# Optimization experiments

Measured on AMD Instinct MI355X. Metric: run time of the kernel, lower is better.

Reference implementation:

```python
import jax, jax.numpy as jnp
import numpy as np

NUM_EDGES = 500_000
FEAT_DIM = 128
TIME_DIM = 100
OUT_DIM = 128
NUM_TYPES = 4


def setup_inputs() -> dict:
    key = jax.random.key(0)
    k1, k2, k3, k4, k5, k6 = jax.random.split(key, 6)
    edge_feats = jax.random.normal(k1, (NUM_EDGES, FEAT_DIM), dtype=jnp.float32)
    edge_ts = jax.random.uniform(k2, (NUM_EDGES,), dtype=jnp.float32) * 100.0
    edge_types = jax.random.randint(k3, (NUM_EDGES,), 0, NUM_TYPES, dtype=jnp.int32)
    # per-type linear encoders: Linear(time_dim + feat_dim, out_dim)
    in_dim = TIME_DIM + FEAT_DIM
    W = jax.random.normal(k4, (NUM_TYPES, in_dim, OUT_DIM), dtype=jnp.float32) * (1.0 / np.sqrt(in_dim))
    b = jax.random.normal(k5, (NUM_TYPES, OUT_DIM), dtype=jnp.float32) * 0.02
    type_emb = jax.random.normal(k6, (NUM_TYPES, OUT_DIM), dtype=jnp.float32)
    # frozen per-type time frequencies: base 1/10**linspace(0,9,T) scaled by (1 + 0.1*i)
    base = (1.0 / 10 ** np.linspace(0, 9, TIME_DIM, dtype=np.float32))
    mult = (1.0 + 0.1 * np.arange(NUM_TYPES, dtype=np.float32))[:, None]
    freqs = jnp.asarray(base[None, :] * mult)  # [T, time_dim]
    return {"edge_feats": edge_feats, "edge_ts": edge_ts, "edge_types": edge_types,
            "W": W, "b": b, "type_emb": type_emb, "freqs": freqs}


def reference(edge_feats, edge_ts, edge_types, W, b, type_emb, freqs):
    # Hetero time encode: cos(t * freq_per_type), bias is zero (frozen)
    time_emb = jnp.cos(edge_ts[:, None] * freqs[edge_types])  # [E, time_dim]
    combined = jnp.concatenate([edge_feats, time_emb], axis=1)  # [E, time+feat]
    num_types = W.shape[0]
    out = jnp.zeros((combined.shape[0], W.shape[2]), dtype=edge_feats.dtype)
    # per-edge-type masked dispatch to separate linear encoders, scatter combine
    for i in range(num_types):
        yi = combined @ W[i] + b[i] + type_emb[i]  # [E, out_dim]
        out = jnp.where((edge_types == i)[:, None], yi, out)
    return out
```

## Files before the change

### kernel.cpp

```cpp
#include <hip/hip_runtime.h>
#include <hip/hip_bf16.h>
#include <cstdint>
#include <cstddef>

#define E_N 500000
#define FD 128
#define TD 100
#define OD 128
#define NT 4
#define IND 228
#define KP 256
#define GX 256
#define NB 1954

static constexpr size_t BUCKET_OFF = 0;
static constexpr size_t WBF_OFF    = 2000000;
static constexpr size_t BIASC_OFF  = WBF_OFF + (size_t)NT * OD * KP * 2;
static constexpr size_t CTR_OFF    = BIASC_OFF + (size_t)NT * OD * 4;
static constexpr size_t PART_OFF   = CTR_OFF + 64;
static constexpr size_t BBASE_OFF  = PART_OFF + (size_t)NB * 4 * 4;
static constexpr size_t WS_NEED    = BBASE_OFF + (size_t)NB * 4 * 4;

typedef __attribute__((ext_vector_type(8))) short short8;
typedef __attribute__((ext_vector_type(4))) float f32x4;

__device__ __forceinline__ unsigned short f2bf(float x) {
  union { float f; unsigned u; } v; v.f = x;
  unsigned r = v.u + 0x7fff + ((v.u >> 16) & 1);
  return (unsigned short)(r >> 16);
}

__device__ __forceinline__ unsigned pack2bf(float a, float b) {
  union { __hip_bfloat162 h; unsigned u; } c;
  c.h = __float22bfloat162_rn(make_float2(a, b));
  return c.u;
}

__device__ __forceinline__ int a_off(int r, int k) {
  return ((r << 9) + (k << 1)) ^ ((r & 7) << 4);
}

__global__ void hist_kernel(const int* __restrict__ types, int* __restrict__ partial, int n) {
  __shared__ int wcnt[4][NT];
  const int tid = threadIdx.x, w = tid >> 6, l = tid & 63;
  const int i = blockIdx.x * 256 + tid;
  const int t = (i < n) ? types[i] : -1;
  #pragma unroll
  for (int q = 0; q < NT; ++q) {
    unsigned long long m = __ballot(t == q);
    if (l == 0) wcnt[w][q] = (int)__popcll(m);
  }
  __syncthreads();
  if (tid < NT) {
    int s = 0;
    #pragma unroll
    for (int w2 = 0; w2 < 4; ++w2) s += wcnt[w2][tid];
    partial[blockIdx.x * NT + tid] = s;
  }
}

__global__ void scan_kernel(const int* __restrict__ partial, int* __restrict__ blockbase,
                            int* __restrict__ ctr, const float* __restrict__ b,
                            const float* __restrict__ temb, float* __restrict__ biasc) {
  __shared__ int4 tsum[256];
  const int tid = threadIdx.x;
  int4 s = make_int4(0, 0, 0, 0);
  #pragma unroll
  for (int j = 0; j < 8; ++j) {
    int blk = tid * 8 + j;
    if (blk < NB) {
      const int* p = partial + blk * 4;
      s.x += p[0]; s.y += p[1]; s.z += p[2]; s.w += p[3];
    }
  }
  tsum[tid] = s;
  __syncthreads();
  if (tid == 0) {
    int4 run = make_int4(0, 0, 0, 0);
    for (int i = 0; i < 256; ++i) {
      int4 v = tsum[i]; tsum[i] = run;
      run.x += v.x; run.y += v.y; run.z += v.z; run.w += v.w;
    }
    ctr[0] = run.x; ctr[1] = run.y; ctr[2] = run.z; ctr[3] = run.w;
    int off = 0;
    ctr[4] = 0;            off += run.x;
    ctr[5] = off;          off += run.y;
    ctr[6] = off;          off += run.z;
    ctr[7] = off;
  }
  __syncthreads();
  int4 run = tsum[tid];
  #pragma unroll
  for (int j = 0; j < 8; ++j) {
    int blk = tid * 8 + j;
    if (blk < NB) {
      const int* p = partial + blk * 4;
      int* bb = blockbase + blk * 4;
      bb[0] = run.x; bb[1] = run.y; bb[2] = run.z; bb[3] = run.w;
      run.x += p[0]; run.y += p[1]; run.z += p[2]; run.w += p[3];
    }
  }
  for (int i = tid; i < NT * OD; i += 256) biasc[i] = b[i] + temb[i];
}

__global__ void wconv_kernel(const float* __restrict__ W, unsigned short* __restrict__ Wbf) {
  int row = blockIdx.x * 4 + (threadIdx.x >> 6);
  int t = row >> 7, n = row & 127;
  int k0 = (threadIdx.x & 63) << 2;
  ushort4 o;
  float v0 = (k0 + 0 < IND) ? W[((size_t)t * IND + k0 + 0) * OD + n] : 0.f;
  float v1 = (k0 + 1 < IND) ? W[((size_t)t * IND + k0 + 1) * OD + n] : 0.f;
  float v2 = (k0 + 2 < IND) ? W[((size_t)t * IND + k0 + 2) * OD + n] : 0.f;
  float v3 = (k0 + 3 < IND) ? W[((size_t)t * IND + k0 + 3) * OD + n] : 0.f;
  o.x = f2bf(v0); o.y = f2bf(v1); o.z = f2bf(v2); o.w = f2bf(v3);
  *(ushort4*)(Wbf + ((size_t)row << 8) + k0) = o;
}

__global__ void fill_kernel(const int* __restrict__ types, const int* __restrict__ blockbase,
                            const int* __restrict__ ctr, int* __restrict__ bucket, int n) {
  __shared__ int wcnt[4][NT];
  __shared__ int wbase[4][NT];
  const int tid = threadIdx.x, w = tid >> 6, l = tid & 63;
  const int i = blockIdx.x * 256 + tid;
  const int t = (i < n) ? types[i] : -1;
  unsigned long long m[NT];
  #pragma unroll
  for (int q = 0; q < NT; ++q) {
    m[q] = __ballot(t == q);
    if (l == 0) wcnt[w][q] = (int)__popcll(m[q]);
  }
  __syncthreads();
  if (tid < NT) {
    int q = tid, s = 0;
    #pragma unroll
    for (int w2 = 0; w2 < 4; ++w2) { wbase[w2][q] = s; s += wcnt[w2][q]; }
  }
  __syncthreads();
  if (t >= 0) {
    int rank = wbase[w][t] + (int)__popcll(m[t] & ((1ull << l) - 1ull));
    bucket[ctr[4 + t] + blockbase[blockIdx.x * 4 + t] + rank] = i;
  }
}

__global__ __launch_bounds__(256) void gemm_kernel(
    const float* __restrict__ feats, const float* __restrict__ ts,
    const float* __restrict__ freqs, const unsigned short* __restrict__ Wbf,
    const float* __restrict__ biasc, const int* __restrict__ bucket,
    const int* __restrict__ ctr, float* __restrict__ out) {
  __shared__ __align__(16) char smA[64 * 512];
  __shared__ __align__(16) float sfreq[128];

  const int t = blockIdx.x;
  const int cnt = ctr[t];
  const int off = ctr[4 + t];
  const int ntiles = (cnt + 63) >> 6;
  const int chunk = (ntiles + GX - 1) / GX;
  const int t0 = blockIdx.y * chunk;
  const int t1 = min(t0 + chunk, ntiles);
  if (t0 >= t1) return;

  const int tid = threadIdx.x;
  const int wid = tid >> 6, lane = tid & 63;
  const int bl = lane & 15, bh = lane >> 4;
  const int r = tid >> 2, part = tid & 3;

  short8 bfrag[8][2];
  #pragma unroll
  for (int n = 0; n < 2; ++n) {
    const unsigned short* bp =
        Wbf + (((size_t)t * OD + wid * 32 + n * 16 + bl) << 8) + (bh << 3);
    #pragma unroll
    for (int k = 0; k < 8; ++k) bfrag[k][n] = *(const short8*)(bp + k * 32);
  }
  const float4 bv0 = *(const float4*)(biasc + t * OD + wid * 32 + bh * 4);
  const float4 bv1 = *(const float4*)(biasc + t * OD + wid * 32 + 16 + bh * 4);

  if (tid < 128) sfreq[tid] = (tid < TD) ? freqs[t * TD + tid] : 0.f;

  auto stage = [&](const float4* p, float tvv) {
    #pragma unroll
    for (int j = 0; j < 4; ++j) {
      uint4 q;
      q.x = pack2bf(p[2 * j].x, p[2 * j].y);
      q.y = pack2bf(p[2 * j].z, p[2 * j].w);
      q.z = pack2bf(p[2 * j + 1].x, p[2 * j + 1].y);
      q.w = pack2bf(p[2 * j + 1].z, p[2 * j + 1].w);
      *(uint4*)(smA + a_off(r, part * 32 + 8 * j)) = q;
    }
    #pragma unroll
    for (int j = 0; j < 4; ++j) {
      float4 f0 = *(const float4*)&sfreq[part * 32 + 8 * j];
      float4 f1 = *(const float4*)&sfreq[part * 32 + 8 * j + 4];
      uint4 q;
      q.x = pack2bf(__cosf(tvv * f0.x), __cosf(tvv * f0.y));
      q.y = pack2bf(__cosf(tvv * f0.z), __cosf(tvv * f0.w));
      q.z = pack2bf(__cosf(tvv * f1.x), __cosf(tvv * f1.y));
      q.w = pack2bf(__cosf(tvv * f1.z), __cosf(tvv * f1.w));
      *(uint4*)(smA + a_off(r, FD + part * 32 + 8 * j)) = q;
    }
  };

  int e_cur = -1; float tv_cur = 0.f;
  {
    const int va = min(64, cnt - t0 * 64);
    if (r < va) { e_cur = bucket[off + t0 * 64 + r]; tv_cur = ts[e_cur]; }
  }
  float4 pf[8];
  if (e_cur >= 0) {
    const float4* src = (const float4*)(feats + (size_t)e_cur * FD + part * 32);
    #pragma unroll
    for (int c = 0; c < 8; ++c) pf[c] = src[c];
  }
  int e_b = -1; float tv_b = 0.f;
  if (t0 + 1 < t1) {
    const int vb = min(64, cnt - (t0 + 1) * 64);
    if (r < vb) { e_b = bucket[off + (t0 + 1) * 64 + r]; tv_b = ts[e_b]; }
  }
  __syncthreads();
  if (e_cur >= 0) stage(pf, tv_cur);

  for (int tt = t0; tt < t1; ++tt) {
    const bool last = (tt == t1 - 1);
    __syncthreads();

    if (!last && e_b >= 0) {
      const float4* src = (const float4*)(feats + (size_t)e_b * FD + part * 32);
      #pragma unroll
      for (int c = 0; c < 8; ++c) pf[c] = src[c];
    }
    int e_c = -1; float tv_c = 0.f;
    if (tt + 2 < t1) {
      const int vc = min(64, cnt - (tt + 2) * 64);
      if (r < vc) { e_c = bucket[off + (tt + 2) * 64 + r]; tv_c = ts[e_c]; }
    }
    const int base = tt * 64;
    const int vcnt = cnt - base;
    int se[4];
    #pragma unroll
    for (int rt = 0; rt < 4; ++rt) {
      int rr = rt * 16 + bl;
      se[rt] = (rr < vcnt) ? bucket[off + base + rr] : -1;
    }

    __builtin_amdgcn_s_setprio(1);
    #pragma unroll
    for (int rt = 0; rt < 4; ++rt) {
      f32x4 a0, a1;
      a0[0] = bv0.x; a0[1] = bv0.y; a0[2] = bv0.z; a0[3] = bv0.w;
      a1[0] = bv1.x; a1[1] = bv1.y; a1[2] = bv1.z; a1[3] = bv1.w;
      #pragma unroll
      for (int k = 0; k < 8; ++k) {
        short8 av = *(const short8*)(smA + a_off(rt * 16 + bl, k * 32 + bh * 8));
        a0 = __builtin_amdgcn_mfma_f32_16x16x32_bf16(bfrag[k][0], av, a0, 0, 0, 0);
        a1 = __builtin_amdgcn_mfma_f32_16x16x32_bf16(bfrag[k][1], av, a1, 0, 0, 0);
      }
      if (se[rt] >= 0) {
        float* dst = out + (size_t)se[rt] * OD + wid * 32 + bh * 4;
        *(f32x4*)(dst)      = a0;
        *(f32x4*)(dst + 16) = a1;
      }
    }
    __builtin_amdgcn_s_setprio(0);
    __syncthreads();

    if (!last) {
      if (e_b >= 0) stage(pf, tv_b);
      e_cur = e_b; tv_cur = tv_b;
      e_b = e_c; tv_b = tv_c;
    }
  }
}

__global__ void naive_kernel(const float* __restrict__ feats, const float* __restrict__ ts,
                             const int* __restrict__ types, const float* __restrict__ W,
                             const float* __restrict__ b, const float* __restrict__ temb,
                             const float* __restrict__ freqs, float* __restrict__ out) {
  __shared__ float comb[IND];
  int e = blockIdx.x;
  int t = types[e];
  int tid = threadIdx.x;
  comb[tid] = feats[(size_t)e * FD + tid];
  if (tid < TD) comb[FD + tid] = __cosf(ts[e] * freqs[t * TD + tid]);
  __syncthreads();
  float acc = b[t * OD + tid] + temb[t * OD + tid];
  for (int k = 0; k < IND; ++k) acc += comb[k] * W[((size_t)t * IND + k) * OD + tid];
  out[(size_t)e * OD + tid] = acc;
}

extern "C" void kernel_launch(void* const* d_in, const int* in_sizes, int n_in,
                              void* d_out, int out_size, void* d_ws, size_t ws_size,
                              hipStream_t stream) {
  const float* feats = (const float*)d_in[0];
  const float* ts    = (const float*)d_in[1];
  const int*   types = (const int*)d_in[2];
  const float* W     = (const float*)d_in[3];
  const float* bb    = (const float*)d_in[4];
  const float* temb  = (const float*)d_in[5];
  const float* freqs = (const float*)d_in[6];
  float* out = (float*)d_out;

  if (ws_size < WS_NEED) {
    naive_kernel<<<E_N, 128, 0, stream>>>(feats, ts, types, W, bb, temb, freqs, out);
    return;
  }

  char* ws = (char*)d_ws;
  int* bucket = (int*)(ws + BUCKET_OFF);
  unsigned short* Wbf = (unsigned short*)(ws + WBF_OFF);
  float* biasc = (float*)(ws + BIASC_OFF);
  int* ctr = (int*)(ws + CTR_OFF);
  int* partial = (int*)(ws + PART_OFF);
  int* blockbase = (int*)(ws + BBASE_OFF);

  hist_kernel<<<NB, 256, 0, stream>>>(types, partial, E_N);
  scan_kernel<<<1, 256, 0, stream>>>(partial, blockbase, ctr, bb, temb, biasc);
  wconv_kernel<<<(NT * OD) / 4, 256, 0, stream>>>(W, Wbf);
  fill_kernel<<<NB, 256, 0, stream>>>(types, blockbase, ctr, bucket, E_N);
  dim3 g(NT, GX);
  gemm_kernel<<<g, 256, 0, stream>>>(feats, ts, freqs, Wbf, biasc, bucket, ctr, out);
}
```

Measured before the change: 151.8 us.

## Double-buffer feature prefetch registers to deepen gather pipeline by one tile

```diff
diff --git a/kernel.cpp b/kernel.cpp
--- a/kernel.cpp
+++ b/kernel.cpp
@@ -200,39 +200,19 @@
     }
   };
 
-  int e_cur = -1; float tv_cur = 0.f;
-  {
-    const int va = min(64, cnt - t0 * 64);
-    if (r < va) { e_cur = bucket[off + t0 * 64 + r]; tv_cur = ts[e_cur]; }
-  }
-  float4 pf[8];
-  if (e_cur >= 0) {
-    const float4* src = (const float4*)(feats + (size_t)e_cur * FD + part * 32);
-    #pragma unroll
-    for (int c = 0; c < 8; ++c) pf[c] = src[c];
-  }
-  int e_b = -1; float tv_b = 0.f;
-  if (t0 + 1 < t1) {
-    const int vb = min(64, cnt - (t0 + 1) * 64);
-    if (r < vb) { e_b = bucket[off + (t0 + 1) * 64 + r]; tv_b = ts[e_b]; }
-  }
-  __syncthreads();
-  if (e_cur >= 0) stage(pf, tv_cur);
-
-  for (int tt = t0; tt < t1; ++tt) {
-    const bool last = (tt == t1 - 1);
-    __syncthreads();
-
-    if (!last && e_b >= 0) {
-      const float4* src = (const float4*)(feats + (size_t)e_b * FD + part * 32);
+  auto fill = [&](int tile, float4* pf, float& tv) -> int {
+    int e = -1;
+    if (tile < t1 && r < cnt - tile * 64) {
+      e = bucket[off + tile * 64 + r];
+      tv = ts[e];
+      const float4* src = (const float4*)(feats + (size_t)e * FD + part * 32);
       #pragma unroll
       for (int c = 0; c < 8; ++c) pf[c] = src[c];
     }
-    int e_c = -1; float tv_c = 0.f;
-    if (tt + 2 < t1) {
-      const int vc = min(64, cnt - (tt + 2) * 64);
-      if (r < vc) { e_c = bucket[off + (tt + 2) * 64 + r]; tv_c = ts[e_c]; }
-    }
+    return e;
+  };
+
+  auto mfma_store = [&](int tt) {
     const int base = tt * 64;
     const int vcnt = cnt - base;
     int se[4];
@@ -241,7 +221,6 @@
       int rr = rt * 16 + bl;
       se[rt] = (rr < vcnt) ? bucket[off + base + rr] : -1;
     }
-
     __builtin_amdgcn_s_setprio(1);
     #pragma unroll
     for (int rt = 0; rt < 4; ++rt) {
@@ -261,13 +240,29 @@
       }
     }
     __builtin_amdgcn_s_setprio(0);
+  };
+
+  float4 pfA[8], pfB[8];
+  float tvA = 0.f, tvB = 0.f;
+  int eA = fill(t0, pfA, tvA);
+  int eB = fill(t0 + 1, pfB, tvB);
+  __syncthreads();
+  if (eA >= 0) stage(pfA, tvA);
+
+  for (int tt = t0; tt < t1; tt += 2) {
     __syncthreads();
-
-    if (!last) {
-      if (e_b >= 0) stage(pf, tv_b);
-      e_cur = e_b; tv_cur = tv_b;
-      e_b = e_c; tv_b = tv_c;
-    }
+    eA = fill(tt + 2, pfA, tvA);
+    mfma_store(tt);
+    __syncthreads();
+    if (tt + 1 >= t1) break;
+    if (eB >= 0) stage(pfB, tvB);
+
+    __syncthreads();
+    eB = fill(tt + 3, pfB, tvB);
+    mfma_store(tt + 1);
+    __syncthreads();
+    if (tt + 2 >= t1) break;
+    if (eA >= 0) stage(pfA, tvA);
   }
 }
 
```

New measurement: 182.0 us. 1.2x slower.
